# Optimization experiments

Hardware: AMD Instinct MI355X
Metric: run time of the kernel (lower is better)

The kernel has to match this reference:

```python
import jax, jax.numpy as jnp
import numpy as np

S, C, HD = 2048, 3072, 128
H = C // HD  # 24 heads
EPS = 1e-6


def setup_inputs() -> dict:
    key = jax.random.key(0)
    ks = jax.random.split(key, 12)
    x = jax.random.normal(ks[0], (S, C), dtype=jnp.float32)
    rope = jax.random.normal(ks[1], (S, 1, HD // 2, 2, 2), dtype=jnp.float32)
    w = 0.02
    return {
        "x": x,
        "rope": rope,
        "wq": jax.random.normal(ks[2], (C, C), dtype=jnp.float32) * w,
        "bq": jnp.zeros((C,), dtype=jnp.float32),
        "wk": jax.random.normal(ks[3], (C, C), dtype=jnp.float32) * w,
        "bk": jnp.zeros((C,), dtype=jnp.float32),
        "wv": jax.random.normal(ks[4], (C, C), dtype=jnp.float32) * w,
        "bv": jnp.zeros((C,), dtype=jnp.float32),
        "wo": jax.random.normal(ks[5], (C, C), dtype=jnp.float32) * w,
        "bo": jnp.zeros((C,), dtype=jnp.float32),
        "qn_w": jnp.ones((HD,), dtype=jnp.float32),
        "kn_w": jnp.ones((HD,), dtype=jnp.float32),
    }


def _rmsnorm(t, w):
    # t: [S, H, HD]; normalize over last dim
    ms = jnp.mean(t * t, axis=-1, keepdims=True)
    return t * jax.lax.rsqrt(ms + EPS) * w


def _apply_rotary(t, rope):
    # t: [S, H, HD] -> [S, H, HD//2, 1, 2]; rope: [S, 1, HD//2, 2, 2]
    t_ = t.reshape(S, H, HD // 2, 1, 2)
    out = jnp.sum(rope * t_, axis=-1)  # [S, H, HD//2, 2]
    return out.reshape(S, H, HD)


def reference(x, rope, wq, bq, wk, bk, wv, bv, wo, bo, qn_w, kn_w):
    q = (x @ wq.T + bq).reshape(S, H, HD)
    k = (x @ wk.T + bk).reshape(S, H, HD)
    v = (x @ wv.T + bv).reshape(S, H, HD)
    q = _rmsnorm(q, qn_w)
    k = _rmsnorm(k, kn_w)
    q = _apply_rotary(q, rope)
    k = _apply_rotary(k, rope)
    # dense SDPA: scores [H, S, S]
    scores = jnp.einsum('shd,thd->hst', q, k) / jnp.sqrt(jnp.float32(HD))
    attn = jax.nn.softmax(scores, axis=-1)
    out = jnp.einsum('hst,thd->shd', attn, v).reshape(S, C)
    return out @ wo.T + bo
```

## Files before the change

### kernel.cpp

```cpp
#include <hip/hip_runtime.h>
#include <cstdint>
#include <cstddef>

#define SS 2048
#define CC 3072
#define HDIM 128
#define NH 24

using bf16 = __bf16;
typedef __bf16 bf16x8 __attribute__((ext_vector_type(8)));
typedef float f32x4 __attribute__((ext_vector_type(4)));

typedef const __attribute__((address_space(1))) void* gas1_cvp;
typedef __attribute__((address_space(3))) void* las3_vp;

__device__ __forceinline__ void gll16(const void* g, void* l) {
  __builtin_amdgcn_global_load_lds((gas1_cvp)g, (las3_vp)l, 16, 0, 0);
}

__device__ __forceinline__ bf16x8 cvt8(f32x4 a, f32x4 b) {
  bf16x8 r;
  r[0] = (bf16)a[0]; r[1] = (bf16)a[1]; r[2] = (bf16)a[2]; r[3] = (bf16)a[3];
  r[4] = (bf16)b[0]; r[5] = (bf16)b[1]; r[6] = (bf16)b[2]; r[7] = (bf16)b[3];
  return r;
}

#define NX ((size_t)SS * CC)
#define NW ((size_t)CC * CC)

__global__ __launch_bounds__(256)
void k_cvt(const float* __restrict__ s0, const float* __restrict__ s1,
           const float* __restrict__ s2, const float* __restrict__ s3,
           const float* __restrict__ s4, bf16* __restrict__ dst) {
  const int z = blockIdx.y;
  const float* src = (z == 0) ? s0 : (z == 1) ? s1 : (z == 2) ? s2 : (z == 3) ? s3 : s4;
  const size_t nz = (z == 0) ? NX : NW;
  const size_t base = (z == 0) ? 0 : NX + (size_t)(z - 1) * NW;
  const size_t i = ((size_t)blockIdx.x * 256 + threadIdx.x) * 8;
  if (i < nz) {
    const f32x4 a = *(const f32x4*)(src + i);
    const f32x4 b = *(const f32x4*)(src + i + 4);
    *(bf16x8*)(dst + base + i) = cvt8(a, b);
  }
}

__device__ __forceinline__ void gemm_bt_bf16(const bf16* __restrict__ A,
                                             const bf16* __restrict__ W,
                                             const float* __restrict__ bias,
                                             void* __restrict__ out,
                                             int M, int N, int K, int mode) {
  __shared__ __align__(16) bf16 As[2][128][32];
  __shared__ __align__(16) bf16 Ws[2][128][32];
  const int t = threadIdx.x, wave = t >> 6, lane = t & 63;
  const int m0 = blockIdx.y * 128, n0 = blockIdx.x * 128;
  const int wm = (wave >> 1) * 64, wn = (wave & 1) * 64;
  const int fr = lane & 15, fq = (lane >> 4) * 8;

  f32x4 acc[4][4] = {};

  for (int k0 = 0; k0 < K; k0 += 64) {
    __syncthreads();
#pragma unroll
    for (int it = 0; it < 4; ++it) {
      const int pc = wave * 4 + it;
      const int pl = pc >> 3, rb = pc & 7;
      const int row = rb * 16 + (lane >> 2);
      const int c8 = (lane & 3) * 8;
      gll16(A + (size_t)(m0 + row) * K + k0 + pl * 32 + c8,
            (char*)&As[0][0][0] + pc * 1024);
      gll16(W + (size_t)(n0 + row) * K + k0 + pl * 32 + c8,
            (char*)&Ws[0][0][0] + pc * 1024);
    }
    __syncthreads();
#pragma unroll
    for (int c = 0; c < 2; ++c) {
      bf16x8 a[4], b[4];
#pragma unroll
      for (int i = 0; i < 4; ++i) a[i] = *(const bf16x8*)&As[c][wm + i * 16 + fr][fq];
#pragma unroll
      for (int j = 0; j < 4; ++j) b[j] = *(const bf16x8*)&Ws[c][wn + j * 16 + fr][fq];
#pragma unroll
      for (int i = 0; i < 4; ++i)
#pragma unroll
        for (int j = 0; j < 4; ++j)
          acc[i][j] = __builtin_amdgcn_mfma_f32_16x16x32_bf16(a[i], b[j], acc[i][j], 0, 0, 0);
    }
  }

  const int lr4 = (lane >> 4) * 4;
#pragma unroll
  for (int i = 0; i < 4; ++i) {
#pragma unroll
    for (int j = 0; j < 4; ++j) {
      const int col = n0 + wn + j * 16 + fr;
      const float bb = bias[col];
#pragma unroll
      for (int r = 0; r < 4; ++r) {
        const int row = m0 + wm + i * 16 + lr4 + r;
        const float v = acc[i][j][r] + bb;
        if (mode == 0)
          ((bf16*)out)[((size_t)(col >> 7) * M + row) * 128 + (col & 127)] = (bf16)v;
        else if (mode == 1)
          ((bf16*)out)[(size_t)col * M + row] = (bf16)v;
        else
          ((float*)out)[(size_t)row * N + col] = v;
      }
    }
  }
}

__global__ __launch_bounds__(256, 4)
void k_gemm_qkv_b(const bf16* __restrict__ xb,
                  const bf16* __restrict__ wqb, const bf16* __restrict__ wkb,
                  const bf16* __restrict__ wvb,
                  const float* __restrict__ bq, const float* __restrict__ bk,
                  const float* __restrict__ bv,
                  bf16* __restrict__ Qo, bf16* __restrict__ Ko, bf16* __restrict__ Vo) {
  const int z = blockIdx.z;
  const bf16* W  = (z == 0) ? wqb : (z == 1) ? wkb : wvb;
  const float* B = (z == 0) ? bq : (z == 1) ? bk : bv;
  void* O        = (z == 0) ? (void*)Qo : (z == 1) ? (void*)Ko : (void*)Vo;
  gemm_bt_bf16(xb, W, B, O, SS, CC, CC, (z == 2) ? 1 : 0);
}

__global__ __launch_bounds__(256, 4)
void k_gemm_out_b(const bf16* __restrict__ A, const bf16* __restrict__ wob,
                  const float* __restrict__ bo, float* __restrict__ out) {
  gemm_bt_bf16(A, wob, bo, out, SS, CC, CC, 2);
}

template<int AF32>
__device__ __forceinline__ void gemm_core(const void* __restrict__ Ap,
                                          const float* __restrict__ W,
                                          const float* __restrict__ bias,
                                          void* __restrict__ out,
                                          int M, int N, int K, int mode) {
  __shared__ __align__(16) bf16 As[128][32];
  __shared__ __align__(16) bf16 Ws[128][32];
  const int t = threadIdx.x, wave = t >> 6, lane = t & 63;
  const int m0 = blockIdx.y * 128, n0 = blockIdx.x * 128;
  const int wm = (wave >> 1) * 64, wn = (wave & 1) * 64;
  const int fr = lane & 15, fq = (lane >> 4) * 8;
  const int pi0 = wave * 128 + lane;
  const int pi1 = pi0 + 64;
  const int row0 = pi0 >> 2, c0 = (pi0 & 3) * 8;
  const int row1 = pi1 >> 2, c1 = (pi1 & 3) * 8;

  f32x4 raf0[2], raf1[2], rw0[2], rw1[2];
  bf16x8 rab0, rab1;

  auto issue = [&](int k0) {
    if (AF32) {
      const float* A = (const float*)Ap;
      const float* p0 = A + (size_t)(m0 + row0) * K + k0 + c0;
      raf0[0] = *(const f32x4*)p0; raf0[1] = *(const f32x4*)(p0 + 4);
      const float* p1 = A + (size_t)(m0 + row1) * K + k0 + c1;
      raf1[0] = *(const f32x4*)p1; raf1[1] = *(const f32x4*)(p1 + 4);
    } else {
      const bf16* A = (const bf16*)Ap;
      rab0 = *(const bf16x8*)(A + (size_t)(m0 + row0) * K + k0 + c0);
      rab1 = *(const bf16x8*)(A + (size_t)(m0 + row1) * K + k0 + c1);
    }
    const float* q0 = W + (size_t)(n0 + row0) * K + k0 + c0;
    rw0[0] = *(const f32x4*)q0; rw0[1] = *(const f32x4*)(q0 + 4);
    const float* q1 = W + (size_t)(n0 + row1) * K + k0 + c1;
    rw1[0] = *(const f32x4*)q1; rw1[1] = *(const f32x4*)(q1 + 4);
  };

  f32x4 acc[4][4] = {};
  issue(0);
  for (int k0 = 0; k0 < K; k0 += 32) {
    __syncthreads();
    if (AF32) {
      *(bf16x8*)&As[row0][c0] = cvt8(raf0[0], raf0[1]);
      *(bf16x8*)&As[row1][c1] = cvt8(raf1[0], raf1[1]);
    } else {
      *(bf16x8*)&As[row0][c0] = rab0;
      *(bf16x8*)&As[row1][c1] = rab1;
    }
    *(bf16x8*)&Ws[row0][c0] = cvt8(rw0[0], rw0[1]);
    *(bf16x8*)&Ws[row1][c1] = cvt8(rw1[0], rw1[1]);
    __syncthreads();
    if (k0 + 32 < K) issue(k0 + 32);
    bf16x8 a[4], b[4];
#pragma unroll
    for (int i = 0; i < 4; ++i) a[i] = *(const bf16x8*)&As[wm + i * 16 + fr][fq];
#pragma unroll
    for (int j = 0; j < 4; ++j) b[j] = *(const bf16x8*)&Ws[wn + j * 16 + fr][fq];
#pragma unroll
    for (int i = 0; i < 4; ++i)
#pragma unroll
      for (int j = 0; j < 4; ++j)
        acc[i][j] = __builtin_amdgcn_mfma_f32_16x16x32_bf16(a[i], b[j], acc[i][j], 0, 0, 0);
  }

  const int lr4 = (lane >> 4) * 4;
#pragma unroll
  for (int i = 0; i < 4; ++i) {
#pragma unroll
    for (int j = 0; j < 4; ++j) {
      const int col = n0 + wn + j * 16 + fr;
      const float bb = bias[col];
#pragma unroll
      for (int r = 0; r < 4; ++r) {
        const int row = m0 + wm + i * 16 + lr4 + r;
        const float v = acc[i][j][r] + bb;
        if (mode == 0)
          ((bf16*)out)[((size_t)(col >> 7) * M + row) * 128 + (col & 127)] = (bf16)v;
        else if (mode == 1)
          ((bf16*)out)[(size_t)col * M + row] = (bf16)v;
        else
          ((float*)out)[(size_t)row * N + col] = v;
      }
    }
  }
}

__global__ __launch_bounds__(256, 2)
void k_gemm_qkv_f(const float* __restrict__ x,
                  const float* __restrict__ wq, const float* __restrict__ wk,
                  const float* __restrict__ wv,
                  const float* __restrict__ bq, const float* __restrict__ bk,
                  const float* __restrict__ bv,
                  bf16* __restrict__ Qo, bf16* __restrict__ Ko, bf16* __restrict__ Vo) {
  const int z = blockIdx.z;
  const float* W = (z == 0) ? wq : (z == 1) ? wk : wv;
  const float* B = (z == 0) ? bq : (z == 1) ? bk : bv;
  void* O        = (z == 0) ? (void*)Qo : (z == 1) ? (void*)Ko : (void*)Vo;
  gemm_core<1>(x, W, B, O, SS, CC, CC, (z == 2) ? 1 : 0);
}

__global__ __launch_bounds__(256, 2)
void k_gemm_out_f(const bf16* __restrict__ A, const float* __restrict__ wo,
                  const float* __restrict__ bo, float* __restrict__ out) {
  gemm_core<0>(A, wo, bo, out, SS, CC, CC, 2);
}

__global__ __launch_bounds__(256)
void k_norm_rope(bf16* __restrict__ Q, bf16* __restrict__ K,
                 const float* __restrict__ rope,
                 const float* __restrict__ qw, const float* __restrict__ kw) {
  const int t = threadIdx.x, wave = t >> 6, lane = t & 63;
  const int idx = blockIdx.x * 4 + wave;
  const int s = idx / NH, h = idx % NH;
  const size_t base = ((size_t)h * SS + s) * HDIM + 2 * lane;

  bf16 q2[2], k2[2];
  *(uint32_t*)q2 = *(const uint32_t*)(Q + base);
  *(uint32_t*)k2 = *(const uint32_t*)(K + base);
  const float q0 = (float)q2[0], q1 = (float)q2[1];
  const float k0 = (float)k2[0], k1 = (float)k2[1];
  float sq = q0 * q0 + q1 * q1;
  float sk = k0 * k0 + k1 * k1;
#pragma unroll
  for (int m = 1; m < 64; m <<= 1) {
    sq += __shfl_xor(sq, m);
    sk += __shfl_xor(sk, m);
  }
  const float rq = rsqrtf(sq * (1.0f / 128.0f) + 1e-6f);
  const float rk = rsqrtf(sk * (1.0f / 128.0f) + 1e-6f);

  const float qn0 = q0 * rq * qw[2 * lane], qn1 = q1 * rq * qw[2 * lane + 1];
  const float kn0 = k0 * rk * kw[2 * lane], kn1 = k1 * rk * kw[2 * lane + 1];

  const f32x4 rp = *(const f32x4*)(rope + (size_t)s * 256 + 4 * lane);
  const float r00 = rp[0], r01 = rp[1], r10 = rp[2], r11 = rp[3];

  const float SC = 0.08838834764831845f * 1.44269504088896340f;
  const float oq0 = (r00 * qn0 + r01 * qn1) * SC;
  const float oq1 = (r10 * qn0 + r11 * qn1) * SC;
  const float ok0 = r00 * kn0 + r01 * kn1;
  const float ok1 = r10 * kn0 + r11 * kn1;

  bf16 wq2[2] = {(bf16)oq0, (bf16)oq1};
  bf16 wk2[2] = {(bf16)ok0, (bf16)ok1};
  *(uint32_t*)(Q + base) = *(uint32_t*)wq2;
  *(uint32_t*)(K + base) = *(uint32_t*)wk2;
}

__global__ __launch_bounds__(128, 2)
void k_attn(const bf16* __restrict__ Q, const bf16* __restrict__ Kt,
            const bf16* __restrict__ Vt, bf16* __restrict__ Out) {
  __shared__ __align__(16) bf16 Ks[64][128];
  __shared__ __align__(16) bf16 Vs[128][64];
  const int t = threadIdx.x, wave = t >> 6, lane = t & 63;
  const int bx = blockIdx.x;
  const int xg = bx & 7, slot = bx >> 3;
  const int h = xg * 3 + (slot >> 5);
  const int q0 = (slot & 31) * 64;
  const int fr = lane & 15, fq = (lane >> 4) * 8;
  const int g4 = lane >> 4;
  const int wq0 = wave * 32;
  const float FM = 32.0f;

  bf16x8 aq[2][4];
#pragma unroll
  for (int qt = 0; qt < 2; ++qt)
#pragma unroll
    for (int kc = 0; kc < 4; ++kc)
      aq[qt][kc] = *(const bf16x8*)(
          Q + ((size_t)h * SS + q0 + wq0 + qt * 16 + fr) * HDIM + kc * 32 + fq);

  f32x4 oacc[2][8] = {};
  float lacc[2] = {0.f, 0.f};

  for (int k0 = 0; k0 < SS; k0 += 64) {
    __syncthreads();
#pragma unroll
    for (int it = 0; it < 8; ++it) {
      const int pc = wave * 8 + it;
      {
        const int s  = pc * 4 + (lane >> 4);
        const int kp = 32 * ((s >> 4) & 1) + 8 * ((s >> 2) & 3)
                     + 4 * (s >> 5) + (s & 3);
        const int sl = (lane & 15) ^ (s & 7);
        gll16(Kt + ((size_t)h * SS + k0 + kp) * HDIM + sl * 8,
              (char*)&Ks[0][0] + pc * 1024);
      }
      {
        const int d  = pc * 8 + (lane >> 3);
        const int sl = (lane & 7) ^ (d & 7);
        gll16(Vt + ((size_t)h * HDIM + d) * SS + k0 + sl * 8,
              (char*)&Vs[0][0] + pc * 1024);
      }
    }
    __syncthreads();

    f32x4 sacc[2][4] = {};
#pragma unroll
    for (int kc = 0; kc < 4; ++kc) {
#pragma unroll
      for (int jt = 0; jt < 4; ++jt) {
        const bf16x8 b =
            *(const bf16x8*)&Ks[jt * 16 + fr][((((kc << 2) + g4) ^ (fr & 7)) << 3)];
        sacc[0][jt] = __builtin_amdgcn_mfma_f32_16x16x32_bf16(b, aq[0][kc], sacc[0][jt], 0, 0, 0);
        sacc[1][jt] = __builtin_amdgcn_mfma_f32_16x16x32_bf16(b, aq[1][kc], sacc[1][jt], 0, 0, 0);
      }
    }

    bf16x8 ap[2][2];
#pragma unroll
    for (int qt = 0; qt < 2; ++qt) {
      float pv[4][4];
      float ps = 0.f;
#pragma unroll
      for (int jt = 0; jt < 4; ++jt)
#pragma unroll
        for (int r = 0; r < 4; ++r) {
          pv[jt][r] = exp2f(sacc[qt][jt][r] - FM);
          ps += pv[jt][r];
        }
      lacc[qt] += ps;
#pragma unroll
      for (int kc = 0; kc < 2; ++kc) {
        bf16x8 a;
        a[0] = (bf16)pv[kc][0];     a[1] = (bf16)pv[kc][1];
        a[2] = (bf16)pv[kc][2];     a[3] = (bf16)pv[kc][3];
        a[4] = (bf16)pv[2 + kc][0]; a[5] = (bf16)pv[2 + kc][1];
        a[6] = (bf16)pv[2 + kc][2]; a[7] = (bf16)pv[2 + kc][3];
        ap[qt][kc] = a;
      }
    }

#pragma unroll
    for (int kc = 0; kc < 2; ++kc) {
#pragma unroll
      for (int jd = 0; jd < 8; ++jd) {
        const int d = jd * 16 + fr;
        const bf16x8 b =
            *(const bf16x8*)&Vs[d][((((kc << 2) + g4) ^ (fr & 7)) << 3)];
        oacc[0][jd] = __builtin_amdgcn_mfma_f32_16x16x32_bf16(ap[0][kc], b, oacc[0][jd], 0, 0, 0);
        oacc[1][jd] = __builtin_amdgcn_mfma_f32_16x16x32_bf16(ap[1][kc], b, oacc[1][jd], 0, 0, 0);
      }
    }
  }

#pragma unroll
  for (int qt = 0; qt < 2; ++qt) {
    float l = lacc[qt];
    l += __shfl_xor(l, 16);
    l += __shfl_xor(l, 32);
    const float linv = 1.0f / l;
#pragma unroll
    for (int r = 0; r < 4; ++r) {
      const float inv = __shfl(linv, g4 * 4 + r, 16);
      const int row = q0 + wq0 + qt * 16 + g4 * 4 + r;
#pragma unroll
      for (int jd = 0; jd < 8; ++jd) {
        const int col = h * HDIM + jd * 16 + fr;
        Out[(size_t)row * CC + col] = (bf16)(oacc[qt][jd][r] * inv);
      }
    }
  }
}

extern "C" void kernel_launch(void* const* d_in, const int* in_sizes, int n_in,
                              void* d_out, int out_size, void* d_ws, size_t ws_size,
                              hipStream_t stream) {
  const float* x    = (const float*)d_in[0];
  const float* rope = (const float*)d_in[1];
  const float* wq   = (const float*)d_in[2];
  const float* bq   = (const float*)d_in[3];
  const float* wk   = (const float*)d_in[4];
  const float* bk   = (const float*)d_in[5];
  const float* wv   = (const float*)d_in[6];
  const float* bv   = (const float*)d_in[7];
  const float* wo   = (const float*)d_in[8];
  const float* bo   = (const float*)d_in[9];
  const float* qw   = (const float*)d_in[10];
  const float* kw   = (const float*)d_in[11];

  const size_t need = (4 * NX + 4 * NW) * sizeof(bf16);
  bf16* Vt = (bf16*)d_out;

  if (ws_size >= need) {
    bf16* xb  = (bf16*)d_ws;
    bf16* wqb = xb + NX;
    bf16* wkb = wqb + NW;
    bf16* wvb = wkb + NW;
    bf16* wob = wvb + NW;
    bf16* Qn  = wob + NW;
    bf16* Kn  = Qn + NX;
    bf16* Ao  = Kn + NX;

    k_cvt<<<dim3((unsigned)(NW / 2048), 5), 256, 0, stream>>>(x, wq, wk, wv, wo, xb);
    k_gemm_qkv_b<<<dim3(CC / 128, SS / 128, 3), 256, 0, stream>>>(
        xb, wqb, wkb, wvb, bq, bk, bv, Qn, Kn, Vt);
    k_norm_rope<<<dim3(SS * NH / 4), 256, 0, stream>>>(Qn, Kn, rope, qw, kw);
    k_attn<<<dim3((SS / 64) * NH), 128, 0, stream>>>(Qn, Kn, Vt, Ao);
    k_gemm_out_b<<<dim3(CC / 128, SS / 128), 256, 0, stream>>>(Ao, wob, bo, (float*)d_out);
  } else {
    bf16* Qn = (bf16*)d_ws;
    bf16* Kn = Qn + NX;
    bf16* Ao = Kn + NX;

    k_gemm_qkv_f<<<dim3(CC / 128, SS / 128, 3), 256, 0, stream>>>(
        x, wq, wk, wv, bq, bk, bv, Qn, Kn, Vt);
    k_norm_rope<<<dim3(SS * NH / 4), 256, 0, stream>>>(Qn, Kn, rope, qw, kw);
    k_attn<<<dim3((SS / 64) * NH), 128, 0, stream>>>(Qn, Kn, Vt, Ao);
    k_gemm_out_f<<<dim3(CC / 128, SS / 128), 256, 0, stream>>>(Ao, wo, bo, (float*)d_out);
  }
}
```

Baseline: 532.0 us.

## Double-buffer K tiles and overlap V load with QK^T in attention

The attention kernel now double-buffers the K tile in LDS, prefetching the next K block while computing the current one. The V load is issued at the start of each iteration and waited on only before the PV matmul, so it overlaps QK^T and softmax. Hand-placed vmcnt waits and raw s_barriers replace the two __syncthreads per tile. LDS use grows by 16KB per block, which may reduce occupancy, and the explicit vmcnt counts must match the issued loads exactly.

```diff
diff --git a/kernel.cpp b/kernel.cpp
--- a/kernel.cpp
+++ b/kernel.cpp
@@ -281,7 +281,7 @@
 __global__ __launch_bounds__(128, 2)
 void k_attn(const bf16* __restrict__ Q, const bf16* __restrict__ Kt,
             const bf16* __restrict__ Vt, bf16* __restrict__ Out) {
-  __shared__ __align__(16) bf16 Ks[64][128];
+  __shared__ __align__(16) bf16 Ks[2][64][128];
   __shared__ __align__(16) bf16 Vs[128][64];
   const int t = threadIdx.x, wave = t >> 6, lane = t & 63;
   const int bx = blockIdx.x;
@@ -301,30 +301,46 @@
       aq[qt][kc] = *(const bf16x8*)(
           Q + ((size_t)h * SS + q0 + wq0 + qt * 16 + fr) * HDIM + kc * 32 + fq);
 
+  auto stageK = [&](int buf, int k0) {
+#pragma unroll
+    for (int it = 0; it < 8; ++it) {
+      const int pc = wave * 8 + it;
+      const int s  = pc * 4 + (lane >> 4);
+      const int kp = 32 * ((s >> 4) & 1) + 8 * ((s >> 2) & 3)
+                   + 4 * (s >> 5) + (s & 3);
+      const int sl = (lane & 15) ^ (s & 7);
+      gll16(Kt + ((size_t)h * SS + k0 + kp) * HDIM + sl * 8,
+            (char*)&Ks[buf][0][0] + pc * 1024);
+    }
+  };
+  auto stageV = [&](int k0) {
+#pragma unroll
+    for (int it = 0; it < 8; ++it) {
+      const int pc = wave * 8 + it;
+      const int d  = pc * 8 + (lane >> 3);
+      const int sl = (lane & 7) ^ (d & 7);
+      gll16(Vt + ((size_t)h * HDIM + d) * SS + k0 + sl * 8,
+            (char*)&Vs[0][0] + pc * 1024);
+    }
+  };
+
   f32x4 oacc[2][8] = {};
   float lacc[2] = {0.f, 0.f};
 
+  stageK(0, 0);
+  int cur = 0;
+
   for (int k0 = 0; k0 < SS; k0 += 64) {
-    __syncthreads();
-#pragma unroll
-    for (int it = 0; it < 8; ++it) {
-      const int pc = wave * 8 + it;
-      {
-        const int s  = pc * 4 + (lane >> 4);
-        const int kp = 32 * ((s >> 4) & 1) + 8 * ((s >> 2) & 3)
-                     + 4 * (s >> 5) + (s & 3);
-        const int sl = (lane & 15) ^ (s & 7);
-        gll16(Kt + ((size_t)h * SS + k0 + kp) * HDIM + sl * 8,
-              (char*)&Ks[0][0] + pc * 1024);
-      }
-      {
-        const int d  = pc * 8 + (lane >> 3);
-        const int sl = (lane & 7) ^ (d & 7);
-        gll16(Vt + ((size_t)h * HDIM + d) * SS + k0 + sl * 8,
-              (char*)&Vs[0][0] + pc * 1024);
-      }
-    }
-    __syncthreads();
+    const bool notlast = (k0 + 64 < SS);
+    stageV(k0);
+    if (notlast) {
+      stageK(cur ^ 1, k0 + 64);
+      asm volatile("s_waitcnt vmcnt(16)" ::: "memory");
+    } else {
+      asm volatile("s_waitcnt vmcnt(8)" ::: "memory");
+    }
+    __builtin_amdgcn_s_barrier();
+    __builtin_amdgcn_sched_barrier(0);
 
     f32x4 sacc[2][4] = {};
 #pragma unroll
@@ -332,7 +348,7 @@
 #pragma unroll
       for (int jt = 0; jt < 4; ++jt) {
         const bf16x8 b =
-            *(const bf16x8*)&Ks[jt * 16 + fr][((((kc << 2) + g4) ^ (fr & 7)) << 3)];
+            *(const bf16x8*)&Ks[cur][jt * 16 + fr][((((kc << 2) + g4) ^ (fr & 7)) << 3)];
         sacc[0][jt] = __builtin_amdgcn_mfma_f32_16x16x32_bf16(b, aq[0][kc], sacc[0][jt], 0, 0, 0);
         sacc[1][jt] = __builtin_amdgcn_mfma_f32_16x16x32_bf16(b, aq[1][kc], sacc[1][jt], 0, 0, 0);
       }
@@ -362,6 +378,14 @@
       }
     }
 
+    if (notlast) {
+      asm volatile("s_waitcnt vmcnt(8)" ::: "memory");
+    } else {
+      asm volatile("s_waitcnt vmcnt(0)" ::: "memory");
+    }
+    __builtin_amdgcn_s_barrier();
+    __builtin_amdgcn_sched_barrier(0);
+
 #pragma unroll
     for (int kc = 0; kc < 2; ++kc) {
 #pragma unroll
@@ -373,6 +397,10 @@
         oacc[1][jd] = __builtin_amdgcn_mfma_f32_16x16x32_bf16(ap[1][kc], b, oacc[1][jd], 0, 0, 0);
       }
     }
+
+    __builtin_amdgcn_s_barrier();
+    __builtin_amdgcn_sched_barrier(0);
+    cur ^= 1;
   }
 
 #pragma unroll
```

New measurement: 508.9 us. 1.05x faster.
